# Performance work log

Hardware: AMD Instinct MI355X
Metric: run time of the kernel (lower is better)

The kernel has to match this reference:

```python
import jax, jax.numpy as jnp
import numpy as np

N, E, H = 100000, 640000, 64
DIN_N, DIN_E, L, OUT = 32, 16, 2, 1
BN_EPS = 1e-5


def setup_inputs() -> dict:
    key = jax.random.key(0)
    ks = iter(jax.random.split(key, 40))
    def p(shape, s=0.05):
        return jax.random.normal(next(ks), shape, dtype=jnp.float32) * s
    return {
        "x": jax.random.normal(next(ks), (N, DIN_N), dtype=jnp.float32),
        "edge_attr": jax.random.normal(next(ks), (E, DIN_E), dtype=jnp.float32),
        "src": jax.random.randint(next(ks), (E,), 0, N),
        "dst": jax.random.randint(next(ks), (E,), 0, N),
        "node_emb_w": p((DIN_N, H)), "node_emb_b": p((H,)),
        "edge_emb_w": p((DIN_E, H)), "edge_emb_b": p((H,)),
        "lin_edge_w": p((L, H, H)), "lin_edge_b": p((L, H)),
        "conv_w1": p((L, H, H)), "conv_b1": p((L, H)),
        "conv_w2": p((L, H, H)), "conv_b2": p((L, H)),
        "emlp_w1": p((L, 3 * H, H)), "emlp_b1": p((L, H)),
        "emlp_w2": p((L, H, H)), "emlp_b2": p((L, H)),
        "bn_gamma": jnp.ones((L, H), jnp.float32),
        "bn_beta": jnp.zeros((L, H), jnp.float32),
        "mlp_w1": p((3 * H, 50)), "mlp_b1": p((50,)),
        "mlp_w2": p((50, 25)), "mlp_b2": p((25,)),
        "mlp_w3": p((25, OUT)), "mlp_b3": p((OUT,)),
    }


def _batchnorm(h, gamma, beta):
    # training-mode BatchNorm1d over the node axis (biased variance)
    mu = jnp.mean(h, axis=0)
    var = jnp.mean(jnp.square(h - mu), axis=0)
    return gamma * (h - mu) * jax.lax.rsqrt(var + BN_EPS) + beta


def _forward(x, edge_attr, src, dst,
             node_emb_w, node_emb_b, edge_emb_w, edge_emb_b,
             lin_edge_w, lin_edge_b, conv_w1, conv_b1, conv_w2, conv_b2,
             emlp_w1, emlp_b1, emlp_w2, emlp_b2, bn_gamma, bn_beta,
             mlp_w1, mlp_b1, mlp_w2, mlp_b2, mlp_w3, mlp_b3):
    x = x @ node_emb_w + node_emb_b                       # [N, H]
    e = edge_attr @ edge_emb_w + edge_emb_b               # [E, H]
    for i in range(L):
        # GINEConv (eps=0): msg = ReLU(x_src + Lin(edge_attr)); sum at dst
        msg = jax.nn.relu(x[src] + e @ lin_edge_w[i] + lin_edge_b[i])
        agg = jax.ops.segment_sum(msg, dst, num_segments=N)
        h = x + agg
        h = jax.nn.relu(h @ conv_w1[i] + conv_b1[i]) @ conv_w2[i] + conv_b2[i]
        x = (x + jax.nn.relu(_batchnorm(h, bn_gamma[i], bn_beta[i]))) / 2
        cat = jnp.concatenate([x[src], x[dst], e], axis=-1)  # [E, 3H]
        upd = jax.nn.relu(cat @ emlp_w1[i] + emlp_b1[i]) @ emlp_w2[i] + emlp_b2[i]
        e = e + upd / 2
    # edge readout: relu(cat(x_src, x_dst)) ++ edge_attr -> MLP (dropout off/eval)
    er = jnp.concatenate(
        [jax.nn.relu(jnp.concatenate([x[src], x[dst]], axis=-1)), e], axis=-1)
    hmid = jax.nn.relu(er @ mlp_w1 + mlp_b1)
    hmid = jax.nn.relu(hmid @ mlp_w2 + mlp_b2)
    logit = hmid @ mlp_w3 + mlp_b3
    return x, logit


def reference(x, edge_attr, src, dst,
              node_emb_w, node_emb_b, edge_emb_w, edge_emb_b,
              lin_edge_w, lin_edge_b, conv_w1, conv_b1, conv_w2, conv_b2,
              emlp_w1, emlp_b1, emlp_w2, emlp_b2, bn_gamma, bn_beta,
              mlp_w1, mlp_b1, mlp_w2, mlp_b2, mlp_w3, mlp_b3):
    return _forward(x, edge_attr, src, dst,
                    node_emb_w, node_emb_b, edge_emb_w, edge_emb_b,
                    lin_edge_w, lin_edge_b, conv_w1, conv_b1, conv_w2, conv_b2,
                    emlp_w1, emlp_b1, emlp_w2, emlp_b2, bn_gamma, bn_beta,
                    mlp_w1, mlp_b1, mlp_w2, mlp_b2, mlp_w3, mlp_b3)
```

## Files before the change

### kernel.cpp

```cpp
#include <hip/hip_runtime.h>

#define NN 100000
#define NE 640000
#define NB_SCAN 98

typedef __attribute__((ext_vector_type(8))) short short8;
typedef __attribute__((ext_vector_type(4))) float f32x4;
typedef __attribute__((ext_vector_type(4))) ushort ushort4v;

__device__ __forceinline__ float bf2f(ushort u) {
    unsigned v = ((unsigned)u) << 16;
    return __builtin_bit_cast(float, v);
}
__device__ __forceinline__ ushort f2bf(float f) {
    unsigned u = __builtin_bit_cast(unsigned, f);
    u += 0x7fffu + ((u >> 16) & 1u);
    return (ushort)(u >> 16);
}
__device__ __forceinline__ short8 brelu(short8 v) {
    #pragma unroll
    for (int i = 0; i < 8; ++i) v[i] = (v[i] < (short)0) ? (short)0 : v[i];
    return v;
}

__global__ void k_hist(const int* __restrict__ dst, int* __restrict__ hist)
{
    int i = blockIdx.x * 256 + threadIdx.x;
    atomicAdd(&hist[dst[i]], 1);
}

__global__ __launch_bounds__(256) void k_scan_part(const int* __restrict__ hist,
                                                   int* __restrict__ rp,
                                                   int* __restrict__ parts)
{
    __shared__ int s[256];
    int b = blockIdx.x, t = threadIdx.x;
    int base = b * 1024 + t * 4;
    int v[4]; int sum = 0;
    #pragma unroll
    for (int i = 0; i < 4; ++i) { int idx = base + i; v[i] = (idx < NN) ? hist[idx] : 0; sum += v[i]; }
    s[t] = sum; __syncthreads();
    for (int off = 1; off < 256; off <<= 1) {
        int x = (t >= off) ? s[t - off] : 0;
        __syncthreads(); s[t] += x; __syncthreads();
    }
    int excl = s[t] - sum;
    if (t == 255) parts[b] = s[255];
    int run = excl;
    #pragma unroll
    for (int i = 0; i < 4; ++i) { int idx = base + i; if (idx < NN) rp[idx] = run; run += v[i]; }
}

__global__ void k_scan_tops(int* __restrict__ parts, int* __restrict__ rp)
{
    __shared__ int s[128];
    int t = threadIdx.x;
    int v = (t < NB_SCAN) ? parts[t] : 0;
    s[t] = v; __syncthreads();
    for (int off = 1; off < 128; off <<= 1) {
        int x = (t >= off) ? s[t - off] : 0;
        __syncthreads(); s[t] += x; __syncthreads();
    }
    parts[t] = s[t] - v;
    if (t == 0) rp[NN] = NE;
}

__global__ __launch_bounds__(256) void k_scan_add(int* __restrict__ rp,
                                                  const int* __restrict__ parts,
                                                  int* __restrict__ cursor)
{
    int i = blockIdx.x * 256 + threadIdx.x;
    if (i >= NN) return;
    int v = rp[i] + parts[i >> 10];
    rp[i] = v; cursor[i] = v;
}

__global__ void k_scatter(const int* __restrict__ src, const int* __restrict__ dst,
                          int* __restrict__ cursor, int* __restrict__ eidx,
                          int* __restrict__ ssrc, int* __restrict__ sdst)
{
    int i = blockIdx.x * 256 + threadIdx.x;
    int d = dst[i];
    int p = atomicAdd(&cursor[d], 1);
    eidx[p] = i; ssrc[p] = src[i]; sdst[p] = d;
}

__global__ void k_w_subtile(const float* __restrict__ w, ushort* __restrict__ out,
                            int K, int Nin)
{
    int t = blockIdx.x * 256 + threadIdx.x;
    if (t >= K * 64) return;
    int k = t >> 6, c = t & 63;
    float v = (c < Nin) ? w[k * Nin + c] : 0.f;
    out[((k >> 3) * 64 + c) * 8 + (k & 7)] = f2bf(v);
}

__global__ void k_w_padk(const float* __restrict__ w, ushort* __restrict__ out,
                         int Kreal, int Kpad)
{
    int t = blockIdx.x * 256 + threadIdx.x;
    if (t >= Kpad * 64) return;
    int k = t >> 6, c = t & 63;
    float v = (k < Kreal) ? w[k * 64 + c] : 0.f;
    out[((k >> 3) * 64 + c) * 8 + (k & 7)] = f2bf(v);
}

__global__ void k_w_msg(const float* __restrict__ lw, ushort* __restrict__ out)
{
    int t = blockIdx.x * 256 + threadIdx.x;
    if (t >= 128 * 64) return;
    int k = t >> 6, c = t & 63;
    float v = (k < 64) ? (k == c ? 1.f : 0.f) : lw[(k - 64) * 64 + c];
    out[((k >> 3) * 64 + c) * 8 + (k & 7)] = f2bf(v);
}

__global__ __launch_bounds__(256) void k_node_emb_mfma(
    const float* __restrict__ xin, const ushort* __restrict__ ws,
    const float* __restrict__ b, float* __restrict__ xout,
    ushort* __restrict__ xb)
{
    __shared__ ushort wl[32 * 64];
    __shared__ float fbuf[4][16 * 64];
    __shared__ ushort bbuf[4][16 * 64];
    int tid = threadIdx.x;
    *(short8*)&wl[tid * 8] = *(const short8*)&ws[tid * 8];
    __syncthreads();

    int wid = tid >> 6, lane = tid & 63, c = lane & 15, kg = lane >> 4;
    int t = blockIdx.x * 4 + wid;
    if (t >= NN / 16) return;
    int n0 = t * 16;

    const float* xr = xin + (size_t)(n0 + c) * 32 + kg * 8;
    f32x4 u0 = *(const f32x4*)xr, u1 = *(const f32x4*)(xr + 4);
    short8 a;
    #pragma unroll
    for (int j = 0; j < 4; ++j) { a[j] = (short)f2bf(u0[j]); a[4 + j] = (short)f2bf(u1[j]); }

    f32x4 acc[4];
    #pragma unroll
    for (int nt = 0; nt < 4; ++nt) {
        float bv = b[nt * 16 + c];
        acc[nt] = f32x4{bv, bv, bv, bv};
        short8 bf = *(const short8*)&wl[(kg * 64 + nt * 16 + c) * 8];
        acc[nt] = __builtin_amdgcn_mfma_f32_16x16x32_bf16(a, bf, acc[nt], 0, 0, 0);
    }
    #pragma unroll
    for (int nt = 0; nt < 4; ++nt)
        #pragma unroll
        for (int i = 0; i < 4; ++i) {
            int rr = kg * 4 + i, cc = nt * 16 + c;
            float v = acc[nt][i];
            fbuf[wid][rr * 64 + cc] = v;
            bbuf[wid][rr * 64 + cc] = f2bf(v);
        }
    #pragma unroll
    for (int r = 0; r < 4; ++r) {
        int q = r * 64 + lane;
        *(f32x4*)&xout[(size_t)(n0 + (q >> 4)) * 64 + (q & 15) * 4] =
            *(f32x4*)&fbuf[wid][q * 4];
    }
    #pragma unroll
    for (int r = 0; r < 2; ++r) {
        int q = r * 64 + lane;
        *(short8*)&xb[(size_t)(n0 + (q >> 3)) * 64 + (q & 7) * 8] =
            *(short8*)&bbuf[wid][q * 8];
    }
}

__global__ __launch_bounds__(256) void k_edge_emb_fused(
    const float* __restrict__ ein, const ushort* __restrict__ ws,
    const float* __restrict__ b, ushort* __restrict__ eb,
    const ushort* __restrict__ xb, const int* __restrict__ ssrc,
    const int* __restrict__ eidx, const ushort* __restrict__ wm,
    const float* __restrict__ lb, ushort* __restrict__ msgbuf)
{
    __shared__ ushort wl[32 * 64];
    __shared__ ushort wml[128 * 64];
    __shared__ ushort bbuf[4][16 * 72];
    int tid = threadIdx.x;
    *(short8*)&wl[tid * 8] = *(const short8*)&ws[tid * 8];
    #pragma unroll
    for (int i = 0; i < 4; ++i)
        *(short8*)&wml[(i * 256 + tid) * 8] = *(const short8*)&wm[(i * 256 + tid) * 8];
    __syncthreads();

    int wid = tid >> 6, lane = tid & 63, c = lane & 15, kg = lane >> 4;
    int p0 = (blockIdx.x * 4 + wid) * 16;
    ushort* bb = bbuf[wid];

    short8 a = (short8)0;
    if (kg < 2) {
        int orig = eidx[p0 + c];
        const float* er = ein + (size_t)orig * 16 + kg * 8;
        f32x4 u0 = *(const f32x4*)er, u1 = *(const f32x4*)(er + 4);
        #pragma unroll
        for (int j = 0; j < 4; ++j) { a[j] = (short)f2bf(u0[j]); a[4 + j] = (short)f2bf(u1[j]); }
    }
    f32x4 acc[4];
    #pragma unroll
    for (int nt = 0; nt < 4; ++nt) {
        float bv = b[nt * 16 + c];
        acc[nt] = f32x4{bv, bv, bv, bv};
        short8 bf = *(const short8*)&wl[(kg * 64 + nt * 16 + c) * 8];
        acc[nt] = __builtin_amdgcn_mfma_f32_16x16x32_bf16(a, bf, acc[nt], 0, 0, 0);
    }
    #pragma unroll
    for (int nt = 0; nt < 4; ++nt)
        #pragma unroll
        for (int i = 0; i < 4; ++i)
            bb[(kg * 4 + i) * 72 + nt * 16 + c] = f2bf(acc[nt][i]);
    #pragma unroll
    for (int r = 0; r < 2; ++r) {
        int q = r * 64 + lane;
        *(short8*)&eb[(size_t)(p0 + (q >> 3)) * 64 + (q & 7) * 8] =
            *(short8*)&bb[(q >> 3) * 72 + (q & 7) * 8];
    }
    short8 en0 = *(const short8*)&bb[c * 72 + kg * 8];
    short8 en1 = *(const short8*)&bb[c * 72 + 32 + kg * 8];
    const ushort* xs = xb + (size_t)ssrc[p0 + c] * 64;
    short8 a0 = *(const short8*)(xs + kg * 8);
    short8 a1 = *(const short8*)(xs + 32 + kg * 8);

    f32x4 acc3[4];
    #pragma unroll
    for (int nt = 0; nt < 4; ++nt) {
        float bv = lb[nt * 16 + c];
        acc3[nt] = f32x4{bv, bv, bv, bv};
    }
    short8 af[4] = {a0, a1, en0, en1};
    #pragma unroll
    for (int ks = 0; ks < 4; ++ks) {
        #pragma unroll
        for (int nt = 0; nt < 4; ++nt) {
            short8 bf = *(const short8*)&wml[((ks * 4 + kg) * 64 + nt * 16 + c) * 8];
            acc3[nt] = __builtin_amdgcn_mfma_f32_16x16x32_bf16(af[ks], bf, acc3[nt], 0, 0, 0);
        }
    }
    #pragma unroll
    for (int nt = 0; nt < 4; ++nt)
        #pragma unroll
        for (int i = 0; i < 4; ++i)
            bb[(kg * 4 + i) * 72 + nt * 16 + c] = f2bf(fmaxf(acc3[nt][i], 0.f));
    #pragma unroll
    for (int r = 0; r < 2; ++r) {
        int q = r * 64 + lane;
        *(short8*)&msgbuf[(size_t)(p0 + (q >> 3)) * 64 + (q & 7) * 8] =
            *(short8*)&bb[(q >> 3) * 72 + (q & 7) * 8];
    }
}

__global__ __launch_bounds__(256) void k_conv_csr(
    const float* __restrict__ x, const ushort* __restrict__ msgbuf,
    const int* __restrict__ rp, float* __restrict__ hout,
    const ushort* __restrict__ w1s, const float* __restrict__ b1,
    const ushort* __restrict__ w2s, const float* __restrict__ b2,
    float* __restrict__ stats)
{
    __shared__ ushort w1l[64 * 64];
    __shared__ ushort w2l[64 * 64];
    __shared__ ushort h1l[4][1024];
    __shared__ float red[2][4][64];
    int tid = threadIdx.x;
    #pragma unroll
    for (int i = 0; i < 2; ++i) {
        *(short8*)&w1l[(i * 256 + tid) * 8] = *(const short8*)&w1s[(i * 256 + tid) * 8];
        *(short8*)&w2l[(i * 256 + tid) * 8] = *(const short8*)&w2s[(i * 256 + tid) * 8];
    }
    __syncthreads();

    int wid = tid >> 6, lane = tid & 63;
    int c = lane & 15, kg = lane >> 4;

    short8 w2f[2][4];
    #pragma unroll
    for (int ks = 0; ks < 2; ++ks)
        #pragma unroll
        for (int nt = 0; nt < 4; ++nt)
            w2f[ks][nt] = *(const short8*)&w2l[((ks * 4 + kg) * 64 + nt * 16 + c) * 8];

    float b1v[4], b2v[4];
    #pragma unroll
    for (int nt = 0; nt < 4; ++nt) { b1v[nt] = b1[nt * 16 + c]; b2v[nt] = b2[nt * 16 + c]; }

    float s1[4] = {0.f, 0.f, 0.f, 0.f}, s2[4] = {0.f, 0.f, 0.f, 0.f};
    ushort* hl = h1l[wid];

    int t = blockIdx.x * 4 + wid;
    if (t < NN / 16) {
        int n0 = t * 16;
        int n = n0 + c;
        int jb = rp[n], je = rp[n + 1];
        float sm0[8] = {0,0,0,0,0,0,0,0}, sm1[8] = {0,0,0,0,0,0,0,0};
        for (int j = jb; j < je; ++j) {
            short8 m0 = *(const short8*)&msgbuf[(size_t)j * 64 + kg * 8];
            short8 m1 = *(const short8*)&msgbuf[(size_t)j * 64 + 32 + kg * 8];
            #pragma unroll
            for (int i = 0; i < 8; ++i) {
                sm0[i] += bf2f((ushort)m0[i]);
                sm1[i] += bf2f((ushort)m1[i]);
            }
        }
        const float* xr = x + (size_t)n * 64;
        f32x4 u0 = *(const f32x4*)(xr + kg * 8);
        f32x4 u1 = *(const f32x4*)(xr + kg * 8 + 4);
        f32x4 v0 = *(const f32x4*)(xr + 32 + kg * 8);
        f32x4 v1 = *(const f32x4*)(xr + 32 + kg * 8 + 4);
        short8 a[2];
        #pragma unroll
        for (int j = 0; j < 4; ++j) {
            a[0][j]     = (short)f2bf(u0[j] + sm0[j]);
            a[0][4 + j] = (short)f2bf(u1[j] + sm0[4 + j]);
            a[1][j]     = (short)f2bf(v0[j] + sm1[j]);
            a[1][4 + j] = (short)f2bf(v1[j] + sm1[4 + j]);
        }
        f32x4 acc[4];
        #pragma unroll
        for (int nt = 0; nt < 4; ++nt) acc[nt] = f32x4{b1v[nt], b1v[nt], b1v[nt], b1v[nt]};
        #pragma unroll
        for (int ks = 0; ks < 2; ++ks) {
            #pragma unroll
            for (int nt = 0; nt < 4; ++nt) {
                short8 bf = *(const short8*)&w1l[((ks * 4 + kg) * 64 + nt * 16 + c) * 8];
                acc[nt] = __builtin_amdgcn_mfma_f32_16x16x32_bf16(a[ks], bf, acc[nt], 0, 0, 0);
            }
        }
        #pragma unroll
        for (int nt = 0; nt < 4; ++nt) {
            #pragma unroll
            for (int i = 0; i < 4; ++i) {
                int rr = kg * 4 + i, cc = nt * 16 + c;
                hl[((cc >> 3) * 16 + rr) * 8 + (cc & 7)] = f2bf(fmaxf(acc[nt][i], 0.f));
            }
        }
        f32x4 acc2[4];
        #pragma unroll
        for (int nt = 0; nt < 4; ++nt) acc2[nt] = f32x4{b2v[nt], b2v[nt], b2v[nt], b2v[nt]};
        #pragma unroll
        for (int ks = 0; ks < 2; ++ks) {
            short8 ha = *(const short8*)&hl[((ks * 4 + kg) * 16 + c) * 8];
            #pragma unroll
            for (int nt = 0; nt < 4; ++nt)
                acc2[nt] = __builtin_amdgcn_mfma_f32_16x16x32_bf16(ha, w2f[ks][nt], acc2[nt], 0, 0, 0);
        }
        #pragma unroll
        for (int nt = 0; nt < 4; ++nt) {
            #pragma unroll
            for (int i = 0; i < 4; ++i) {
                int rr = kg * 4 + i, cc = nt * 16 + c;
                float h2 = acc2[nt][i];
                hout[(size_t)(n0 + rr) * 64 + cc] = h2;
                s1[nt] += h2;
                s2[nt] += h2 * h2;
            }
        }
    }
    #pragma unroll
    for (int nt = 0; nt < 4; ++nt) {
        float v1 = s1[nt], v2 = s2[nt];
        v1 += __shfl_xor(v1, 16); v1 += __shfl_xor(v1, 32);
        v2 += __shfl_xor(v2, 16); v2 += __shfl_xor(v2, 32);
        s1[nt] = v1; s2[nt] = v2;
    }
    if (lane < 16) {
        #pragma unroll
        for (int nt = 0; nt < 4; ++nt) {
            red[0][wid][nt * 16 + c] = s1[nt];
            red[1][wid][nt * 16 + c] = s2[nt];
        }
    }
    __syncthreads();
    if (wid == 0) {
        float a = red[0][0][lane] + red[0][1][lane] + red[0][2][lane] + red[0][3][lane];
        float b = red[1][0][lane] + red[1][1][lane] + red[1][2][lane] + red[1][3][lane];
        unsafeAtomicAdd(&stats[lane], a);
        unsafeAtomicAdd(&stats[64 + lane], b);
    }
}

__global__ void k_bnfin(float* __restrict__ stats,
                        const float* __restrict__ gamma,
                        const float* __restrict__ beta)
{
    int j = threadIdx.x;
    float mu = stats[j] * (1.f / NN);
    float var = stats[64 + j] * (1.f / NN) - mu * mu;
    float a = gamma[j] * rsqrtf(var + 1e-5f);
    stats[128 + j] = a;
    stats[192 + j] = beta[j] - mu * a;
}

__global__ __launch_bounds__(256) void k_xupd4(float* __restrict__ x,
                                               const float* __restrict__ h,
                                               const float* __restrict__ stats,
                                               ushort* __restrict__ xb)
{
    int idx = blockIdx.x * 256 + threadIdx.x;
    int j4 = (idx & 15) * 4;
    f32x4 hv = *(const f32x4*)&h[(size_t)idx * 4];
    f32x4 xv = *(const f32x4*)&x[(size_t)idx * 4];
    f32x4 av = *(const f32x4*)&stats[128 + j4];
    f32x4 cv = *(const f32x4*)&stats[192 + j4];
    f32x4 xo;
    ushort4v bo;
    #pragma unroll
    for (int i = 0; i < 4; ++i) {
        float r = fmaxf(fmaf(hv[i], av[i], cv[i]), 0.f);
        float xn = (xv[i] + r) * 0.5f;
        xo[i] = xn;
        bo[i] = f2bf(xn);
    }
    *(f32x4*)&x[(size_t)idx * 4] = xo;
    *(ushort4v*)&xb[(size_t)idx * 4] = bo;
}

template<int NEXT>
__global__ __launch_bounds__(512) void k_emlp_fused(
    const ushort* __restrict__ xb, ushort* __restrict__ eb,
    const int* __restrict__ ssrc, const int* __restrict__ sdst,
    const ushort* __restrict__ w1s, const float* __restrict__ b1,
    const ushort* __restrict__ w2s, const float* __restrict__ b2,
    const ushort* __restrict__ wm, const float* __restrict__ lbn,
    ushort* __restrict__ msgbuf)
{
    __shared__ ushort w1l[192 * 64];
    __shared__ ushort wml[NEXT ? 128 * 64 : 8];
    __shared__ ushort hb[8][1152];
    int tid = threadIdx.x;
    #pragma unroll
    for (int i = 0; i < 3; ++i)
        *(short8*)&w1l[(i * 512 + tid) * 8] = *(const short8*)&w1s[(i * 512 + tid) * 8];
    if (NEXT) {
        #pragma unroll
        for (int i = 0; i < 2; ++i)
            *(short8*)&wml[(i * 512 + tid) * 8] = *(const short8*)&wm[(i * 512 + tid) * 8];
    }
    __syncthreads();

    int wid = tid >> 6, lane = tid & 63;
    int c = lane & 15, kg = lane >> 4;

    short8 w2f[2][4];
    #pragma unroll
    for (int ks = 0; ks < 2; ++ks)
        #pragma unroll
        for (int nt = 0; nt < 4; ++nt)
            w2f[ks][nt] = *(const short8*)&w2s[((ks * 4 + kg) * 64 + nt * 16 + c) * 8];

    float b1v[4], b2v[4], lbv[4];
    #pragma unroll
    for (int nt = 0; nt < 4; ++nt) {
        b1v[nt] = b1[nt * 16 + c];
        b2v[nt] = b2[nt * 16 + c];
        lbv[nt] = NEXT ? lbn[nt * 16 + c] : 0.f;
    }
    ushort* hl = hb[wid];

    #pragma unroll 1
    for (int t4 = 0; t4 < 4; ++t4) {
        int p0 = blockIdx.x * 512 + wid * 64 + t4 * 16;
        int myp = p0 + c;
        int s = ssrc[myp], d = sdst[myp];
        const ushort* xs = xb + (size_t)s * 64;
        const ushort* xd = xb + (size_t)d * 64;
        const ushort* ee = eb + (size_t)myp * 64;
        short8 a[6];
        a[0] = *(const short8*)(xs + kg * 8);
        a[1] = *(const short8*)(xs + 32 + kg * 8);
        a[2] = *(const short8*)(xd + kg * 8);
        a[3] = *(const short8*)(xd + 32 + kg * 8);
        a[4] = *(const short8*)(ee + kg * 8);
        a[5] = *(const short8*)(ee + 32 + kg * 8);

        f32x4 acc[4];
        #pragma unroll
        for (int nt = 0; nt < 4; ++nt) acc[nt] = f32x4{b1v[nt], b1v[nt], b1v[nt], b1v[nt]};
        #pragma unroll
        for (int ks = 0; ks < 6; ++ks) {
            #pragma unroll
            for (int nt = 0; nt < 4; ++nt) {
                short8 bf = *(const short8*)&w1l[((ks * 4 + kg) * 64 + nt * 16 + c) * 8];
                acc[nt] = __builtin_amdgcn_mfma_f32_16x16x32_bf16(a[ks], bf, acc[nt], 0, 0, 0);
            }
        }
        #pragma unroll
        for (int nt = 0; nt < 4; ++nt) {
            #pragma unroll
            for (int i = 0; i < 4; ++i) {
                int rr = kg * 4 + i, cc = nt * 16 + c;
                hl[((cc >> 3) * 16 + rr) * 8 + (cc & 7)] = f2bf(fmaxf(acc[nt][i], 0.f));
            }
        }
        f32x4 acc2[4];
        #pragma unroll
        for (int nt = 0; nt < 4; ++nt) acc2[nt] = f32x4{b2v[nt], b2v[nt], b2v[nt], b2v[nt]};
        #pragma unroll
        for (int ks = 0; ks < 2; ++ks) {
            short8 ha = *(const short8*)&hl[((ks * 4 + kg) * 16 + c) * 8];
            #pragma unroll
            for (int nt = 0; nt < 4; ++nt)
                acc2[nt] = __builtin_amdgcn_mfma_f32_16x16x32_bf16(ha, w2f[ks][nt], acc2[nt], 0, 0, 0);
        }
        #pragma unroll
        for (int nt = 0; nt < 4; ++nt)
            #pragma unroll
            for (int i = 0; i < 4; ++i)
                hl[(kg * 4 + i) * 72 + nt * 16 + c] = f2bf(acc2[nt][i]);
        short8 u0 = *(const short8*)&hl[c * 72 + kg * 8];
        short8 u1 = *(const short8*)&hl[c * 72 + 32 + kg * 8];
        short8 en0, en1;
        #pragma unroll
        for (int j = 0; j < 8; ++j) {
            en0[j] = (short)f2bf(bf2f((ushort)a[4][j]) + 0.5f * bf2f((ushort)u0[j]));
            en1[j] = (short)f2bf(bf2f((ushort)a[5][j]) + 0.5f * bf2f((ushort)u1[j]));
        }
        *(short8*)&eb[(size_t)myp * 64 + kg * 8]      = en0;
        *(short8*)&eb[(size_t)myp * 64 + 32 + kg * 8] = en1;

        if (NEXT) {
            f32x4 acc3[4];
            #pragma unroll
            for (int nt = 0; nt < 4; ++nt) acc3[nt] = f32x4{lbv[nt], lbv[nt], lbv[nt], lbv[nt]};
            short8 af[4] = {a[0], a[1], en0, en1};
            #pragma unroll
            for (int ks = 0; ks < 4; ++ks) {
                #pragma unroll
                for (int nt = 0; nt < 4; ++nt) {
                    short8 bf = *(const short8*)&wml[((ks * 4 + kg) * 64 + nt * 16 + c) * 8];
                    acc3[nt] = __builtin_amdgcn_mfma_f32_16x16x32_bf16(af[ks], bf, acc3[nt], 0, 0, 0);
                }
            }
            #pragma unroll
            for (int nt = 0; nt < 4; ++nt)
                #pragma unroll
                for (int i = 0; i < 4; ++i)
                    hl[(kg * 4 + i) * 72 + nt * 16 + c] = f2bf(fmaxf(acc3[nt][i], 0.f));
            #pragma unroll
            for (int r = 0; r < 2; ++r) {
                int q = r * 64 + lane;
                *(short8*)&msgbuf[(size_t)(p0 + (q >> 3)) * 64 + (q & 7) * 8] =
                    *(short8*)&hl[(q >> 3) * 72 + (q & 7) * 8];
            }
        }
    }
}

__global__ __launch_bounds__(256) void k_readout_mfma(
    const ushort* __restrict__ xb, const ushort* __restrict__ eb,
    const int* __restrict__ ssrc, const int* __restrict__ sdst,
    const int* __restrict__ eidx,
    const ushort* __restrict__ w1s, const float* __restrict__ b1,
    const float* __restrict__ w2, const float* __restrict__ b2,
    const float* __restrict__ w3, const float* __restrict__ b3,
    float* __restrict__ logit)
{
    __shared__ ushort w1l[192 * 64];
    __shared__ ushort hw[4][64 * 50];
    int tid = threadIdx.x;
    #pragma unroll
    for (int i = 0; i < 6; ++i)
        *(short8*)&w1l[(i * 256 + tid) * 8] = *(const short8*)&w1s[(i * 256 + tid) * 8];
    __syncthreads();

    int wid = tid >> 6, lane = tid & 63;
    int c = lane & 15, kg = lane >> 4;
    float b1v[4];
    #pragma unroll
    for (int nt = 0; nt < 4; ++nt) b1v[nt] = (nt * 16 + c < 50) ? b1[nt * 16 + c] : 0.f;

    #pragma unroll 1
    for (int t4 = 0; t4 < 4; ++t4) {
        int p0 = blockIdx.x * 256 + wid * 64 + t4 * 16;
        int myp = p0 + c;
        int s = ssrc[myp], d = sdst[myp];
        const ushort* xs = xb + (size_t)s * 64;
        const ushort* xd = xb + (size_t)d * 64;
        const ushort* ee = eb + (size_t)myp * 64;
        short8 a[6];
        a[0] = brelu(*(const short8*)(xs + kg * 8));
        a[1] = brelu(*(const short8*)(xs + 32 + kg * 8));
        a[2] = brelu(*(const short8*)(xd + kg * 8));
        a[3] = brelu(*(const short8*)(xd + 32 + kg * 8));
        a[4] = *(const short8*)(ee + kg * 8);
        a[5] = *(const short8*)(ee + 32 + kg * 8);

        f32x4 acc[4];
        #pragma unroll
        for (int nt = 0; nt < 4; ++nt) acc[nt] = f32x4{b1v[nt], b1v[nt], b1v[nt], b1v[nt]};
        #pragma unroll
        for (int ks = 0; ks < 6; ++ks) {
            #pragma unroll
            for (int nt = 0; nt < 4; ++nt) {
                short8 bf = *(const short8*)&w1l[((ks * 4 + kg) * 64 + nt * 16 + c) * 8];
                acc[nt] = __builtin_amdgcn_mfma_f32_16x16x32_bf16(a[ks], bf, acc[nt], 0, 0, 0);
            }
        }
        #pragma unroll
        for (int nt = 0; nt < 4; ++nt) {
            #pragma unroll
            for (int i = 0; i < 4; ++i) {
                int rr = kg * 4 + i, cc = nt * 16 + c;
                if (cc < 50)
                    hw[wid][(t4 * 16 + rr) * 50 + cc] = f2bf(fmaxf(acc[nt][i], 0.f));
            }
        }
    }
    int p = blockIdx.x * 256 + wid * 64 + lane;
    const ushort* hrow = &hw[wid][lane * 50];
    float a25[25];
    #pragma unroll
    for (int j = 0; j < 25; ++j) a25[j] = b2[j];
    #pragma unroll 2
    for (int k = 0; k < 50; ++k) {
        float hv = bf2f(hrow[k]);
        #pragma unroll
        for (int j = 0; j < 25; ++j) a25[j] = fmaf(hv, w2[k * 25 + j], a25[j]);
    }
    float lg = b3[0];
    #pragma unroll
    for (int k = 0; k < 25; ++k) lg = fmaf(fmaxf(a25[k], 0.f), w3[k], lg);
    logit[eidx[p]] = lg;
}

extern "C" void kernel_launch(void* const* d_in, const int* in_sizes, int n_in,
                              void* d_out, int out_size, void* d_ws, size_t ws_size,
                              hipStream_t stream)
{
    const float* x_in  = (const float*)d_in[0];
    const float* eattr = (const float*)d_in[1];
    const int*   src   = (const int*)d_in[2];
    const int*   dst   = (const int*)d_in[3];
    const float* n_w   = (const float*)d_in[4];
    const float* n_b   = (const float*)d_in[5];
    const float* e_w   = (const float*)d_in[6];
    const float* e_b   = (const float*)d_in[7];
    const float* lw    = (const float*)d_in[8];
    const float* lb    = (const float*)d_in[9];
    const float* cw1   = (const float*)d_in[10];
    const float* cb1   = (const float*)d_in[11];
    const float* cw2   = (const float*)d_in[12];
    const float* cb2   = (const float*)d_in[13];
    const float* ew1   = (const float*)d_in[14];
    const float* eb1   = (const float*)d_in[15];
    const float* ew2   = (const float*)d_in[16];
    const float* eb2   = (const float*)d_in[17];
    const float* gam   = (const float*)d_in[18];
    const float* bet   = (const float*)d_in[19];
    const float* m1w   = (const float*)d_in[20];
    const float* m1b   = (const float*)d_in[21];
    const float* m2w   = (const float*)d_in[22];
    const float* m2b   = (const float*)d_in[23];
    const float* m3w   = (const float*)d_in[24];
    const float* m3b   = (const float*)d_in[25];

    float* xbuf  = (float*)d_out;
    float* logit = xbuf + (size_t)NN * 64;

    ushort* eb     = (ushort*)d_ws;
    float*  tmp    = (float*)(eb + (size_t)NE * 64);
    float*  stats  = tmp + (size_t)NN * 64;
    ushort* w1s    = (ushort*)(stats + 256);
    ushort* w2s    = w1s + 2 * 192 * 64;
    ushort* m1s    = w2s + 2 * 64 * 64;
    ushort* xb     = m1s + 192 * 64;
    ushort* wms    = xb + (size_t)NN * 64;
    ushort* cw1s   = wms + 2 * 128 * 64;
    ushort* cw2s   = cw1s + 2 * 64 * 64;
    ushort* nws    = cw2s + 2 * 64 * 64;
    ushort* ews    = nws + 32 * 64;
    ushort* msgbuf = ews + 32 * 64;
    int*    hist   = (int*)(msgbuf + (size_t)NE * 64);
    int*    rp     = hist + NN;
    int*    cursor = rp + NN + 1;
    int*    parts  = cursor + NN;
    int*    eidx   = parts + 128;
    int*    ssrc   = eidx + NE;
    int*    sdst   = ssrc + NE;

    hipMemsetAsync(hist, 0, NN * sizeof(int), stream);
    k_hist<<<NE / 256, 256, 0, stream>>>(dst, hist);
    k_scan_part<<<NB_SCAN, 256, 0, stream>>>(hist, rp, parts);
    k_scan_tops<<<1, 128, 0, stream>>>(parts, rp);
    k_scan_add<<<(NN + 255) / 256, 256, 0, stream>>>(rp, parts, cursor);
    k_scatter<<<NE / 256, 256, 0, stream>>>(src, dst, cursor, eidx, ssrc, sdst);

    k_w_subtile<<<48, 256, 0, stream>>>(ew1,            w1s,            192, 64);
    k_w_subtile<<<48, 256, 0, stream>>>(ew1 + 192 * 64, w1s + 192 * 64, 192, 64);
    k_w_subtile<<<16, 256, 0, stream>>>(ew2,            w2s,            64, 64);
    k_w_subtile<<<16, 256, 0, stream>>>(ew2 + 64 * 64,  w2s + 64 * 64,  64, 64);
    k_w_subtile<<<48, 256, 0, stream>>>(m1w,            m1s,            192, 50);
    k_w_msg<<<32, 256, 0, stream>>>(lw,           wms);
    k_w_msg<<<32, 256, 0, stream>>>(lw + 64 * 64, wms + 128 * 64);
    k_w_subtile<<<16, 256, 0, stream>>>(cw1,            cw1s,           64, 64);
    k_w_subtile<<<16, 256, 0, stream>>>(cw1 + 64 * 64,  cw1s + 64 * 64, 64, 64);
    k_w_subtile<<<16, 256, 0, stream>>>(cw2,            cw2s,           64, 64);
    k_w_subtile<<<16, 256, 0, stream>>>(cw2 + 64 * 64,  cw2s + 64 * 64, 64, 64);
    k_w_padk<<<8, 256, 0, stream>>>(n_w, nws, 32, 32);
    k_w_padk<<<8, 256, 0, stream>>>(e_w, ews, 16, 32);

    k_node_emb_mfma<<<(NN / 16 + 3) / 4, 256, 0, stream>>>(x_in, nws, n_b, xbuf, xb);
    k_edge_emb_fused<<<NE / 64, 256, 0, stream>>>(eattr, ews, e_b, eb,
                                                  xb, ssrc, eidx, wms, lb, msgbuf);

    for (int l = 0; l < 2; ++l) {
        hipMemsetAsync(stats, 0, 256 * sizeof(float), stream);
        k_conv_csr<<<(NN / 16 + 3) / 4, 256, 0, stream>>>(
            xbuf, msgbuf, rp, tmp, cw1s + l * 64 * 64, cb1 + l * 64,
            cw2s + l * 64 * 64, cb2 + l * 64, stats);
        k_bnfin<<<1, 64, 0, stream>>>(stats, gam + l * 64, bet + l * 64);
        k_xupd4<<<NN * 16 / 256, 256, 0, stream>>>(xbuf, tmp, stats, xb);
        if (l == 0) {
            k_emlp_fused<1><<<NE / 512, 512, 0, stream>>>(
                xb, eb, ssrc, sdst, w1s, eb1, w2s, eb2,
                wms + 128 * 64, lb + 64, msgbuf);
        } else {
            k_emlp_fused<0><<<NE / 512, 512, 0, stream>>>(
                xb, eb, ssrc, sdst, w1s + 192 * 64, eb1 + 64, w2s + 64 * 64, eb2 + 64,
                wms, lb, msgbuf);
        }
    }

    k_readout_mfma<<<NE / 256, 256, 0, stream>>>(xb, eb, ssrc, sdst, eidx,
                                                 m1s, m1b, m2w, m2b, m3w, m3b, logit);
}
```

Before: 626.9 us.

## Prefetch next edge tile gathers and shrink emlp blocks to 256 threads

The emlp and readout kernels now software-pipeline their per-wave loop: the gathered x_src, x_dst and edge rows for the next 16-edge tile are loaded before the current tile's MFMAs, so gather latency overlaps compute. The emlp kernel moves from 512-thread to 256-thread blocks, halving its shared scratch and doubling the grid. The edge-embed kernel issues its x_src gather earlier, and the per-layer stats memset is replaced by one up-front memset of two separate stats buffers. The trade-off is higher register pressure from the prefetch buffers, which may lower occupancy, and each smaller emlp block still reloads the full weights into shared memory.

Measured after the change: 556.2 us. -11.3%, faster.

```diff
diff --git a/kernel.cpp b/kernel.cpp
--- a/kernel.cpp
+++ b/kernel.cpp
@@ -189,6 +189,10 @@
     int p0 = (blockIdx.x * 4 + wid) * 16;
     ushort* bb = bbuf[wid];
 
+    const ushort* xs = xb + (size_t)ssrc[p0 + c] * 64;
+    short8 a0 = *(const short8*)(xs + kg * 8);
+    short8 a1 = *(const short8*)(xs + 32 + kg * 8);
+
     short8 a = (short8)0;
     if (kg < 2) {
         int orig = eidx[p0 + c];
@@ -218,9 +222,6 @@
     }
     short8 en0 = *(const short8*)&bb[c * 72 + kg * 8];
     short8 en1 = *(const short8*)&bb[c * 72 + 32 + kg * 8];
-    const ushort* xs = xb + (size_t)ssrc[p0 + c] * 64;
-    short8 a0 = *(const short8*)(xs + kg * 8);
-    short8 a1 = *(const short8*)(xs + 32 + kg * 8);
 
     f32x4 acc3[4];
     #pragma unroll
@@ -415,7 +416,7 @@
 }
 
 template<int NEXT>
-__global__ __launch_bounds__(512) void k_emlp_fused(
+__global__ __launch_bounds__(256) void k_emlp_fused(
     const ushort* __restrict__ xb, ushort* __restrict__ eb,
     const int* __restrict__ ssrc, const int* __restrict__ sdst,
     const ushort* __restrict__ w1s, const float* __restrict__ b1,
@@ -425,15 +426,15 @@
 {
     __shared__ ushort w1l[192 * 64];
     __shared__ ushort wml[NEXT ? 128 * 64 : 8];
-    __shared__ ushort hb[8][1152];
+    __shared__ ushort hb[4][1152];
     int tid = threadIdx.x;
     #pragma unroll
-    for (int i = 0; i < 3; ++i)
-        *(short8*)&w1l[(i * 512 + tid) * 8] = *(const short8*)&w1s[(i * 512 + tid) * 8];
+    for (int i = 0; i < 6; ++i)
+        *(short8*)&w1l[(i * 256 + tid) * 8] = *(const short8*)&w1s[(i * 256 + tid) * 8];
     if (NEXT) {
         #pragma unroll
-        for (int i = 0; i < 2; ++i)
-            *(short8*)&wml[(i * 512 + tid) * 8] = *(const short8*)&wm[(i * 512 + tid) * 8];
+        for (int i = 0; i < 4; ++i)
+            *(short8*)&wml[(i * 256 + tid) * 8] = *(const short8*)&wm[(i * 256 + tid) * 8];
     }
     __syncthreads();
 
@@ -456,21 +457,42 @@
     }
     ushort* hl = hb[wid];
 
-    #pragma unroll 1
-    for (int t4 = 0; t4 < 4; ++t4) {
-        int p0 = blockIdx.x * 512 + wid * 64 + t4 * 16;
-        int myp = p0 + c;
+    int pbase = blockIdx.x * 256 + wid * 64;
+
+    short8 a[6];
+    {
+        int myp = pbase + c;
         int s = ssrc[myp], d = sdst[myp];
         const ushort* xs = xb + (size_t)s * 64;
         const ushort* xd = xb + (size_t)d * 64;
         const ushort* ee = eb + (size_t)myp * 64;
-        short8 a[6];
         a[0] = *(const short8*)(xs + kg * 8);
         a[1] = *(const short8*)(xs + 32 + kg * 8);
         a[2] = *(const short8*)(xd + kg * 8);
         a[3] = *(const short8*)(xd + 32 + kg * 8);
         a[4] = *(const short8*)(ee + kg * 8);
         a[5] = *(const short8*)(ee + 32 + kg * 8);
+    }
+
+    #pragma unroll 1
+    for (int t4 = 0; t4 < 4; ++t4) {
+        int p0 = pbase + t4 * 16;
+        int myp = p0 + c;
+
+        short8 an[6];
+        if (t4 < 3) {
+            int sn = ssrc[myp + 16];
+            int dn = sdst[myp + 16];
+            const ushort* xsn = xb + (size_t)sn * 64;
+            const ushort* xdn = xb + (size_t)dn * 64;
+            const ushort* een = eb + (size_t)(myp + 16) * 64;
+            an[0] = *(const short8*)(xsn + kg * 8);
+            an[1] = *(const short8*)(xsn + 32 + kg * 8);
+            an[2] = *(const short8*)(xdn + kg * 8);
+            an[3] = *(const short8*)(xdn + 32 + kg * 8);
+            an[4] = *(const short8*)(een + kg * 8);
+            an[5] = *(const short8*)(een + 32 + kg * 8);
+        }
 
         f32x4 acc[4];
         #pragma unroll
@@ -541,6 +563,11 @@
                 *(short8*)&msgbuf[(size_t)(p0 + (q >> 3)) * 64 + (q & 7) * 8] =
                     *(short8*)&hl[(q >> 3) * 72 + (q & 7) * 8];
             }
+        }
+
+        if (t4 < 3) {
+            #pragma unroll
+            for (int i = 0; i < 6; ++i) a[i] = an[i];
         }
     }
 }
@@ -568,21 +595,47 @@
     #pragma unroll
     for (int nt = 0; nt < 4; ++nt) b1v[nt] = (nt * 16 + c < 50) ? b1[nt * 16 + c] : 0.f;
 
-    #pragma unroll 1
-    for (int t4 = 0; t4 < 4; ++t4) {
-        int p0 = blockIdx.x * 256 + wid * 64 + t4 * 16;
-        int myp = p0 + c;
+    int pbase = blockIdx.x * 256 + wid * 64;
+
+    short8 a[6];
+    {
+        int myp = pbase + c;
         int s = ssrc[myp], d = sdst[myp];
         const ushort* xs = xb + (size_t)s * 64;
         const ushort* xd = xb + (size_t)d * 64;
         const ushort* ee = eb + (size_t)myp * 64;
-        short8 a[6];
-        a[0] = brelu(*(const short8*)(xs + kg * 8));
-        a[1] = brelu(*(const short8*)(xs + 32 + kg * 8));
-        a[2] = brelu(*(const short8*)(xd + kg * 8));
-        a[3] = brelu(*(const short8*)(xd + 32 + kg * 8));
+        a[0] = *(const short8*)(xs + kg * 8);
+        a[1] = *(const short8*)(xs + 32 + kg * 8);
+        a[2] = *(const short8*)(xd + kg * 8);
+        a[3] = *(const short8*)(xd + 32 + kg * 8);
         a[4] = *(const short8*)(ee + kg * 8);
         a[5] = *(const short8*)(ee + 32 + kg * 8);
+    }
+
+    #pragma unroll 1
+    for (int t4 = 0; t4 < 4; ++t4) {
+        int p0 = pbase + t4 * 16;
+        int myp = p0 + c;
+
+        short8 an[6];
+        if (t4 < 3) {
+            int sn = ssrc[myp + 16];
+            int dn = sdst[myp + 16];
+            const ushort* xsn = xb + (size_t)sn * 64;
+            const ushort* xdn = xb + (size_t)dn * 64;
+            const ushort* een = eb + (size_t)(myp + 16) * 64;
+            an[0] = *(const short8*)(xsn + kg * 8);
+            an[1] = *(const short8*)(xsn + 32 + kg * 8);
+            an[2] = *(const short8*)(xdn + kg * 8);
+            an[3] = *(const short8*)(xdn + 32 + kg * 8);
+            an[4] = *(const short8*)(een + kg * 8);
+            an[5] = *(const short8*)(een + 32 + kg * 8);
+        }
+
+        short8 af[6];
+        af[0] = brelu(a[0]); af[1] = brelu(a[1]);
+        af[2] = brelu(a[2]); af[3] = brelu(a[3]);
+        af[4] = a[4];        af[5] = a[5];
 
         f32x4 acc[4];
         #pragma unroll
@@ -592,7 +645,7 @@
             #pragma unroll
             for (int nt = 0; nt < 4; ++nt) {
                 short8 bf = *(const short8*)&w1l[((ks * 4 + kg) * 64 + nt * 16 + c) * 8];
-                acc[nt] = __builtin_amdgcn_mfma_f32_16x16x32_bf16(a[ks], bf, acc[nt], 0, 0, 0);
+                acc[nt] = __builtin_amdgcn_mfma_f32_16x16x32_bf16(af[ks], bf, acc[nt], 0, 0, 0);
             }
         }
         #pragma unroll
@@ -604,8 +657,12 @@
                     hw[wid][(t4 * 16 + rr) * 50 + cc] = f2bf(fmaxf(acc[nt][i], 0.f));
             }
         }
-    }
-    int p = blockIdx.x * 256 + wid * 64 + lane;
+        if (t4 < 3) {
+            #pragma unroll
+            for (int i = 0; i < 6; ++i) a[i] = an[i];
+        }
+    }
+    int p = pbase + lane;
     const ushort* hrow = &hw[wid][lane * 50];
     float a25[25];
     #pragma unroll
@@ -659,7 +716,7 @@
     ushort* eb     = (ushort*)d_ws;
     float*  tmp    = (float*)(eb + (size_t)NE * 64);
     float*  stats  = tmp + (size_t)NN * 64;
-    ushort* w1s    = (ushort*)(stats + 256);
+    ushort* w1s    = (ushort*)(stats + 512);
     ushort* w2s    = w1s + 2 * 192 * 64;
     ushort* m1s    = w2s + 2 * 64 * 64;
     ushort* xb     = m1s + 192 * 64;
@@ -678,6 +735,7 @@
     int*    sdst   = ssrc + NE;
 
     hipMemsetAsync(hist, 0, NN * sizeof(int), stream);
+    hipMemsetAsync(stats, 0, 512 * sizeof(float), stream);
     k_hist<<<NE / 256, 256, 0, stream>>>(dst, hist);
     k_scan_part<<<NB_SCAN, 256, 0, stream>>>(hist, rp, parts);
     k_scan_tops<<<1, 128, 0, stream>>>(parts, rp);
@@ -703,18 +761,18 @@
                                                   xb, ssrc, eidx, wms, lb, msgbuf);
 
     for (int l = 0; l < 2; ++l) {
-        hipMemsetAsync(stats, 0, 256 * sizeof(float), stream);
+        float* st = stats + l * 256;
         k_conv_csr<<<(NN / 16 + 3) / 4, 256, 0, stream>>>(
             xbuf, msgbuf, rp, tmp, cw1s + l * 64 * 64, cb1 + l * 64,
-            cw2s + l * 64 * 64, cb2 + l * 64, stats);
-        k_bnfin<<<1, 64, 0, stream>>>(stats, gam + l * 64, bet + l * 64);
-        k_xupd4<<<NN * 16 / 256, 256, 0, stream>>>(xbuf, tmp, stats, xb);
+            cw2s + l * 64 * 64, cb2 + l * 64, st);
+        k_bnfin<<<1, 64, 0, stream>>>(st, gam + l * 64, bet + l * 64);
+        k_xupd4<<<NN * 16 / 256, 256, 0, stream>>>(xbuf, tmp, st, xb);
         if (l == 0) {
-            k_emlp_fused<1><<<NE / 512, 512, 0, stream>>>(
+            k_emlp_fused<1><<<NE / 256, 256, 0, stream>>>(
                 xb, eb, ssrc, sdst, w1s, eb1, w2s, eb2,
                 wms + 128 * 64, lb + 64, msgbuf);
         } else {
-            k_emlp_fused<0><<<NE / 512, 512, 0, stream>>>(
+            k_emlp_fused<0><<<NE / 256, 256, 0, stream>>>(
                 xb, eb, ssrc, sdst, w1s + 192 * 64, eb1 + 64, w2s + 64 * 64, eb2 + 64,
                 wms, lb, msgbuf);
         }
```
